# Kernel optimization log

Hardware: AMD Instinct MI355X
Metric: run time of the kernel (lower is better)

## Reference

```python
import jax, jax.numpy as jnp
import numpy as np

OUT_FEATURES = 4096
IN_FEATURES = 4096
GROUP_SIZE = 32
NUM_GROUPS = (OUT_FEATURES * IN_FEATURES) // GROUP_SIZE  # 524288, divisible by 8
PACKED_PER_GROUP = GROUP_SIZE * 3 // 8  # 12


def dequantize_3bit(x_packed, maxvals):
    # x_packed: [NUM_GROUPS * 12] int, values in [0,256) (uint8 bit patterns)
    # maxvals:  [NUM_GROUPS] float32 group scales
    G = NUM_GROUPS
    # view as [G, 4, 3]: 4 byte-triplets per group, each encoding 8 3-bit values
    p = x_packed.reshape(G, GROUP_SIZE // 8, 3)
    b0, b1, b2 = p[..., 0], p[..., 1], p[..., 2]
    v0 = b0 & 7
    v1 = (b0 >> 3) & 7
    v2 = ((b0 >> 6) & 3) | ((b1 & 1) << 2)
    v3 = (b1 >> 1) & 7
    v4 = (b1 >> 4) & 7
    v5 = ((b1 >> 7) & 1) | ((b2 & 3) << 1)
    v6 = (b2 >> 2) & 7
    v7 = (b2 >> 5) & 7
    q = jnp.stack([v0, v1, v2, v3, v4, v5, v6, v7], axis=-1)  # [G, 4, 8]
    q = q.reshape(G, GROUP_SIZE).astype(jnp.float32)
    x_norm = (q / 7.0 * 2.0 - 1.0) * maxvals[:, None]
    return x_norm.reshape(-1)  # [G * GROUP_SIZE]


def setup_inputs() -> dict:
    key = jax.random.key(0)
    k1, k2, k3, k4 = jax.random.split(key, 4)
    x = jax.random.normal(k1, (2, 2048, IN_FEATURES), dtype=jnp.float32)
    weight_q3 = jax.random.randint(k2, (NUM_GROUPS * PACKED_PER_GROUP,), 0, 256, dtype=jnp.int32)
    weight_norm = jax.random.uniform(k3, (NUM_GROUPS,), dtype=jnp.float32)
    bias = jax.random.normal(k4, (OUT_FEATURES,), dtype=jnp.float32)
    return {"x": x, "weight_q3": weight_q3, "weight_norm": weight_norm, "bias": bias}


def reference(x, weight_q3, weight_norm, bias):
    w_flat = dequantize_3bit(weight_q3, weight_norm)
    weight = w_flat[: OUT_FEATURES * IN_FEATURES].reshape(OUT_FEATURES, IN_FEATURES)
    # F.linear: y = x @ W.T + b
    return jnp.einsum("bsi,oi->bso", x, weight) + bias
```

## Files before the change

### kernel.cpp

```cpp
#include <hip/hip_runtime.h>

typedef unsigned short u16;
typedef unsigned int u32;

typedef __bf16 bf16x8 __attribute__((ext_vector_type(8)));
typedef float f32x4 __attribute__((ext_vector_type(4)));

#define OUT_F 4096
#define IN_F 4096
#define M_ROWS 4096
#define NUM_GROUPS ((OUT_F * IN_F) / 32)

#define TILE_E (256 * 64)


__device__ __forceinline__ u16 f2bf(float f) {
    union { float f; u32 u; } c; c.f = f;
    u32 u = c.u;
    u += 0x7fffu + ((u >> 16) & 1u);
    return (u16)(u >> 16);
}

__device__ __forceinline__ u32 pk2(float a, float b) {
    return (u32)f2bf(a) | ((u32)f2bf(b) << 16);
}

__device__ __forceinline__ void async_copy16(const u16* g, u16* l) {
    __builtin_amdgcn_global_load_lds(
        (const __attribute__((address_space(1))) u32*)g,
        (__attribute__((address_space(3))) u32*)l,
        16, 0, 0);
}

__device__ __forceinline__ u32 lds_addr(const u16* p) {
    return (u32)(uintptr_t)(const __attribute__((address_space(3))) u16*)p;
}

__global__ __launch_bounds__(256) void prep_kernel(
        const float* __restrict__ x, const int* __restrict__ q,
        const float* __restrict__ scales,
        u16* __restrict__ W, u16* __restrict__ Xb) {
    int bid = blockIdx.x;
    int tid = threadIdx.x;
    if (bid < 8192) {
        int t = bid * 256 + tid;
        int b0 = q[3 * t];
        int b1 = q[3 * t + 1];
        int b2 = q[3 * t + 2];
        float mv = scales[t >> 2];
        float s = mv * (2.0f / 7.0f);
        float o = -mv;

        int v0 = b0 & 7;
        int v1 = (b0 >> 3) & 7;
        int v2 = ((b0 >> 6) & 3) | ((b1 & 1) << 2);
        int v3 = (b1 >> 1) & 7;
        int v4 = (b1 >> 4) & 7;
        int v5 = ((b1 >> 7) & 1) | ((b2 & 3) << 1);
        int v6 = (b2 >> 2) & 7;
        int v7 = (b2 >> 5) & 7;
        uint4 w;
        w.x = pk2(fmaf((float)v0, s, o), fmaf((float)v1, s, o));
        w.y = pk2(fmaf((float)v2, s, o), fmaf((float)v3, s, o));
        w.z = pk2(fmaf((float)v4, s, o), fmaf((float)v5, s, o));
        w.w = pk2(fmaf((float)v6, s, o), fmaf((float)v7, s, o));
        ((uint4*)W)[t] = w;
    } else {
        int i = (bid - 8192) * 256 + tid;
        const float4* p = (const float4*)x + (size_t)i * 2;
        float4 u = p[0], v = p[1];
        uint4 w;
        w.x = pk2(u.x, u.y);
        w.y = pk2(u.z, u.w);
        w.z = pk2(v.x, v.y);
        w.w = pk2(v.z, v.w);
        ((uint4*)Xb)[i] = w;
    }
}

__global__ __launch_bounds__(512, 2) void gemm_bt_kernel(
        const u16* __restrict__ A, const u16* __restrict__ B,
        const float* __restrict__ bias, float* __restrict__ C) {
    __shared__ u16 sA[2 * TILE_E];
    __shared__ u16 sB[2 * TILE_E];

    const int tid = threadIdx.x;
    const int lane = tid & 63;
    const int w = tid >> 6;
    const int wr = w >> 2;
    const int wc = w & 3;
    const int ln = lane & 15;
    const int quad = lane >> 4;
    const int lnx = ln & 7;

    const int lin = blockIdx.x;
    const int wg = (lin & 7) * 32 + (lin >> 3);
    const int mb = (wg >> 4) * 256;
    const int nb = (wg & 15) * 256;

    int offg[2], offl[2];
#pragma unroll
    for (int p = 0; p < 2; ++p) {
        int s = p * 512 + tid;
        int rl = s >> 3, pc = s & 7;
        int lc = pc ^ (rl & 7);
        offg[p] = rl * IN_F + lc * 8;
        offl[p] = rl * 64 + pc * 8;
    }
    const u16* baseA = A + (size_t)mb * IN_F;
    const u16* baseB = B + (size_t)nb * IN_F;

    auto STAGE = [&](u16* lbase, const u16* gbase, int ko, int h) {
#pragma unroll
        for (int p = 0; p < 2; ++p)
            async_copy16(gbase + h * (128 * IN_F) + offg[p] + ko,
                         lbase + h * (128 * 64) + offl[p]);
    };

    const u32 sAb = lds_addr(sA);
    const u32 sBb = lds_addr(sB);
    const u32 aB0 = sAb + (u32)(wr * 8192 + ln * 128 + ((quad ^ lnx) * 16));
    const u32 aB1 = sAb + (u32)(wr * 8192 + ln * 128 + (((4 + quad) ^ lnx) * 16));
    const u32 bB0 = sBb + (u32)(wc * 4096 + ln * 128 + ((quad ^ lnx) * 16));
    const u32 bB1 = sBb + (u32)(wc * 4096 + ln * 128 + (((4 + quad) ^ lnx) * 16));

    float bj[2][2];
#pragma unroll
    for (int nh = 0; nh < 2; ++nh)
#pragma unroll
        for (int j = 0; j < 2; ++j)
            bj[nh][j] = bias[nb + nh * 128 + wc * 32 + j * 16 + ln];

    f32x4 acc[8][4];
#pragma unroll
    for (int i = 0; i < 8; ++i)
#pragma unroll
        for (int j = 0; j < 4; ++j) acc[i][j] = (f32x4)0.0f;

    bf16x8 av[4][2];
    bf16x8 bv0[2][2];
    bf16x8 bv1[2][2];

#define DSR(dst, base, IMM) \
    asm volatile("ds_read_b128 %0, %1 offset:" #IMM \
                 : "=v"(dst) : "v"(base))

#define WAITG(N) \
    asm volatile("s_waitcnt lgkmcnt(" #N ")"); \
    __builtin_amdgcn_sched_barrier(0);

#define MG(AI, ACR, J0, J1, BV) \
    acc[ACR][J0] = __builtin_amdgcn_mfma_f32_16x16x32_bf16( \
        av[AI][0], BV[0][0], acc[ACR][J0], 0, 0, 0); \
    acc[ACR][J0] = __builtin_amdgcn_mfma_f32_16x16x32_bf16( \
        av[AI][1], BV[0][1], acc[ACR][J0], 0, 0, 0); \
    acc[ACR][J1] = __builtin_amdgcn_mfma_f32_16x16x32_bf16( \
        av[AI][0], BV[1][0], acc[ACR][J1], 0, 0, 0); \
    acc[ACR][J1] = __builtin_amdgcn_mfma_f32_16x16x32_bf16( \
        av[AI][1], BV[1][1], acc[ACR][J1], 0, 0, 0);

    STAGE(sA, baseA, 0, 0);
    STAGE(sA, baseA, 0, 1);
    STAGE(sB, baseB, 0, 0);
    STAGE(sB, baseB, 0, 1);
    asm volatile("s_waitcnt vmcnt(0)");
    __builtin_amdgcn_s_barrier();

#pragma unroll 1
    for (int t = 0; t < 64; ++t) {
        const int cur = t & 1;
        const u32 curOff = (u32)cur << 15;
        const u32 aC0 = aB0 + curOff, aC1 = aB1 + curOff;
        const u32 bC0 = bB0 + curOff, bC1 = bB1 + curOff;
        u16* aNx = sA + (cur ^ 1) * TILE_E;
        u16* bNx = sB + (cur ^ 1) * TILE_E;
        const int ko1 = ((t + 1) & 63) << 6;

        DSR(bv0[0][0], bC0, 0);      DSR(bv0[0][1], bC1, 0);
        DSR(bv0[1][0], bC0, 2048);   DSR(bv0[1][1], bC1, 2048);
        DSR(av[0][0], aC0, 0);       DSR(av[0][1], aC1, 0);
        DSR(av[1][0], aC0, 2048);    DSR(av[1][1], aC1, 2048);
        DSR(av[2][0], aC0, 4096);    DSR(av[2][1], aC1, 4096);
        DSR(av[3][0], aC0, 6144);    DSR(av[3][1], aC1, 6144);
        DSR(bv1[0][0], bC0, 16384);  DSR(bv1[0][1], bC1, 16384);
        DSR(bv1[1][0], bC0, 18432);  DSR(bv1[1][1], bC1, 18432);

        STAGE(aNx, baseA, ko1, 0);
        STAGE(aNx, baseA, ko1, 1);
        STAGE(bNx, baseB, ko1, 0);
        STAGE(bNx, baseB, ko1, 1);
        __builtin_amdgcn_sched_barrier(0);

        __builtin_amdgcn_s_setprio(1);
        WAITG(10); MG(0, 0, 0, 1, bv0);
        WAITG(8);  MG(1, 1, 0, 1, bv0);
        WAITG(6);  MG(2, 2, 0, 1, bv0);
        WAITG(4);  MG(3, 3, 0, 1, bv0);
        WAITG(0);
        MG(0, 0, 2, 3, bv1);
        MG(1, 1, 2, 3, bv1);
        MG(2, 2, 2, 3, bv1);
        MG(3, 3, 2, 3, bv1);
        __builtin_amdgcn_sched_barrier(0);
        __builtin_amdgcn_s_setprio(0);

        DSR(av[0][0], aC0, 16384);   DSR(av[0][1], aC1, 16384);
        DSR(av[1][0], aC0, 18432);   DSR(av[1][1], aC1, 18432);
        DSR(av[2][0], aC0, 20480);   DSR(av[2][1], aC1, 20480);
        DSR(av[3][0], aC0, 22528);   DSR(av[3][1], aC1, 22528);

        __builtin_amdgcn_s_setprio(1);
        WAITG(6); MG(0, 4, 2, 3, bv1);
        WAITG(4); MG(1, 5, 2, 3, bv1);
        WAITG(2); MG(2, 6, 2, 3, bv1);
        WAITG(0); MG(3, 7, 2, 3, bv1);
        MG(0, 4, 0, 1, bv0);
        MG(1, 5, 0, 1, bv0);
        MG(2, 6, 0, 1, bv0);
        MG(3, 7, 0, 1, bv0);
        __builtin_amdgcn_sched_barrier(0);
        __builtin_amdgcn_s_setprio(0);

        asm volatile("s_waitcnt vmcnt(0)");
        __builtin_amdgcn_s_barrier();
    }

#undef DSR
#undef WAITG
#undef MG

    asm volatile("s_waitcnt vmcnt(0)");

#pragma unroll
    for (int ai = 0; ai < 8; ++ai) {
        const int mh = ai >> 2, i = ai & 3;
        const int mrow = mb + mh * 128 + wr * 64 + i * 16 + quad * 4;
#pragma unroll
        for (int j4 = 0; j4 < 4; ++j4) {
            const int nh = j4 >> 1, j = j4 & 1;
            const int col = nb + nh * 128 + wc * 32 + j * 16 + ln;
            float* cp = C + (size_t)mrow * OUT_F + col;
#pragma unroll
            for (int r = 0; r < 4; ++r)
                cp[(size_t)r * OUT_F] = acc[ai][j4][r] + bj[nh][j];
        }
    }
}

extern "C" void kernel_launch(void* const* d_in, const int* in_sizes, int n_in,
                              void* d_out, int out_size, void* d_ws, size_t ws_size,
                              hipStream_t stream) {
    const float* x = (const float*)d_in[0];
    const int* wq = (const int*)d_in[1];
    const float* wn = (const float*)d_in[2];
    const float* bias = (const float*)d_in[3];
    float* out = (float*)d_out;

    u16* Wb = (u16*)d_ws;
    u16* Xb = Wb + (size_t)OUT_F * IN_F;

    prep_kernel<<<16384, 256, 0, stream>>>(x, wq, wn, Wb, Xb);
    gemm_bt_kernel<<<dim3(256), 512, 0, stream>>>(Xb, Wb, bias, out);
}
```

Measured before the change: 141.3 us.

## Switch GEMM inner loop from 16x16x32 to 32x32x16 bf16 MFMA tiles

Replaces the 16x16x32 MFMA micro-tiles with 32x32x16 MFMA instructions. Each wave now owns a contiguous 128x64 output block as 4x2 accumulators of 16 floats. The LDS read addressing is rewritten to match the existing XOR swizzle, and K is processed in four 16-wide steps using two ping-pong register sets. The aim is fewer LDS reads per FLOP, since each 32x32 fragment gets more reuse, and fewer MFMA issues. The cost is a different store pattern in the epilogue and a risk of LDS bank conflicts or changed register pressure.

```diff
diff --git a/kernel.cpp b/kernel.cpp
--- a/kernel.cpp
+++ b/kernel.cpp
@@ -4,7 +4,7 @@
 typedef unsigned int u32;
 
 typedef __bf16 bf16x8 __attribute__((ext_vector_type(8)));
-typedef float f32x4 __attribute__((ext_vector_type(4)));
+typedef float f32x16 __attribute__((ext_vector_type(16)));
 
 #define OUT_F 4096
 #define IN_F 4096
@@ -89,9 +89,11 @@
     const int w = tid >> 6;
     const int wr = w >> 2;
     const int wc = w & 3;
-    const int ln = lane & 15;
-    const int quad = lane >> 4;
-    const int lnx = ln & 7;
+    const int l31 = lane & 31;
+    const int hi = lane >> 5;
+    const int l7 = lane & 7;
+    const int l72 = (l7 >> 1) & 3;
+    const int lb0 = l7 & 1;
 
     const int lin = blockIdx.x;
     const int wg = (lin & 7) * 32 + (lin >> 3);
@@ -119,27 +121,28 @@
 
     const u32 sAb = lds_addr(sA);
     const u32 sBb = lds_addr(sB);
-    const u32 aB0 = sAb + (u32)(wr * 8192 + ln * 128 + ((quad ^ lnx) * 16));
-    const u32 aB1 = sAb + (u32)(wr * 8192 + ln * 128 + (((4 + quad) ^ lnx) * 16));
-    const u32 bB0 = sBb + (u32)(wc * 4096 + ln * 128 + ((quad ^ lnx) * 16));
-    const u32 bB1 = sBb + (u32)(wc * 4096 + ln * 128 + (((4 + quad) ^ lnx) * 16));
-
-    float bj[2][2];
-#pragma unroll
-    for (int nh = 0; nh < 2; ++nh)
-#pragma unroll
-        for (int j = 0; j < 2; ++j)
-            bj[nh][j] = bias[nb + nh * 128 + wc * 32 + j * 16 + ln];
-
-    f32x4 acc[8][4];
-#pragma unroll
-    for (int i = 0; i < 8; ++i)
-#pragma unroll
-        for (int j = 0; j < 4; ++j) acc[i][j] = (f32x4)0.0f;
-
-    bf16x8 av[4][2];
-    bf16x8 bv0[2][2];
-    bf16x8 bv1[2][2];
+    const u32 aS = sAb + (u32)((wr * 128 + l31) * 128 + 16 * (hi ^ lb0));
+    const u32 bS = sBb + (u32)((wc * 64 + l31) * 128 + 16 * (hi ^ lb0));
+    u32 aK[4], bK[4];
+#pragma unroll
+    for (int ks = 0; ks < 4; ++ks) {
+        aK[ks] = aS + (u32)(32 * (ks ^ l72));
+        bK[ks] = bS + (u32)(32 * (ks ^ l72));
+    }
+
+    float bj[2];
+#pragma unroll
+    for (int cb = 0; cb < 2; ++cb)
+        bj[cb] = bias[nb + wc * 64 + cb * 32 + l31];
+
+    f32x16 acc[4][2];
+#pragma unroll
+    for (int rb = 0; rb < 4; ++rb)
+#pragma unroll
+        for (int cb = 0; cb < 2; ++cb) acc[rb][cb] = (f32x16)0.0f;
+
+    bf16x8 avE[4], bvE[2];
+    bf16x8 avO[4], bvO[2];
 
 #define DSR(dst, base, IMM) \
     asm volatile("ds_read_b128 %0, %1 offset:" #IMM \
@@ -149,15 +152,20 @@
     asm volatile("s_waitcnt lgkmcnt(" #N ")"); \
     __builtin_amdgcn_sched_barrier(0);
 
-#define MG(AI, ACR, J0, J1, BV) \
-    acc[ACR][J0] = __builtin_amdgcn_mfma_f32_16x16x32_bf16( \
-        av[AI][0], BV[0][0], acc[ACR][J0], 0, 0, 0); \
-    acc[ACR][J0] = __builtin_amdgcn_mfma_f32_16x16x32_bf16( \
-        av[AI][1], BV[0][1], acc[ACR][J0], 0, 0, 0); \
-    acc[ACR][J1] = __builtin_amdgcn_mfma_f32_16x16x32_bf16( \
-        av[AI][0], BV[1][0], acc[ACR][J1], 0, 0, 0); \
-    acc[ACR][J1] = __builtin_amdgcn_mfma_f32_16x16x32_bf16( \
-        av[AI][1], BV[1][1], acc[ACR][J1], 0, 0, 0);
+#define MFMA_K(AV, BV) \
+    acc[0][0] = __builtin_amdgcn_mfma_f32_32x32x16_bf16(AV[0], BV[0], acc[0][0], 0, 0, 0); \
+    acc[1][0] = __builtin_amdgcn_mfma_f32_32x32x16_bf16(AV[1], BV[0], acc[1][0], 0, 0, 0); \
+    acc[2][0] = __builtin_amdgcn_mfma_f32_32x32x16_bf16(AV[2], BV[0], acc[2][0], 0, 0, 0); \
+    acc[3][0] = __builtin_amdgcn_mfma_f32_32x32x16_bf16(AV[3], BV[0], acc[3][0], 0, 0, 0); \
+    acc[0][1] = __builtin_amdgcn_mfma_f32_32x32x16_bf16(AV[0], BV[1], acc[0][1], 0, 0, 0); \
+    acc[1][1] = __builtin_amdgcn_mfma_f32_32x32x16_bf16(AV[1], BV[1], acc[1][1], 0, 0, 0); \
+    acc[2][1] = __builtin_amdgcn_mfma_f32_32x32x16_bf16(AV[2], BV[1], acc[2][1], 0, 0, 0); \
+    acc[3][1] = __builtin_amdgcn_mfma_f32_32x32x16_bf16(AV[3], BV[1], acc[3][1], 0, 0, 0);
+
+#define READ_K(AV, BV, AT, BT) \
+    DSR(AV[0], AT, 0);  DSR(AV[1], AT, 4096); \
+    DSR(AV[2], AT, 8192); DSR(AV[3], AT, 12288); \
+    DSR(BV[0], BT, 0);  DSR(BV[1], BT, 4096);
 
     STAGE(sA, baseA, 0, 0);
     STAGE(sA, baseA, 0, 1);
@@ -170,20 +178,16 @@
     for (int t = 0; t < 64; ++t) {
         const int cur = t & 1;
         const u32 curOff = (u32)cur << 15;
-        const u32 aC0 = aB0 + curOff, aC1 = aB1 + curOff;
-        const u32 bC0 = bB0 + curOff, bC1 = bB1 + curOff;
+        const u32 aT0 = aK[0] + curOff, aT1 = aK[1] + curOff;
+        const u32 aT2 = aK[2] + curOff, aT3 = aK[3] + curOff;
+        const u32 bT0 = bK[0] + curOff, bT1 = bK[1] + curOff;
+        const u32 bT2 = bK[2] + curOff, bT3 = bK[3] + curOff;
         u16* aNx = sA + (cur ^ 1) * TILE_E;
         u16* bNx = sB + (cur ^ 1) * TILE_E;
         const int ko1 = ((t + 1) & 63) << 6;
 
-        DSR(bv0[0][0], bC0, 0);      DSR(bv0[0][1], bC1, 0);
-        DSR(bv0[1][0], bC0, 2048);   DSR(bv0[1][1], bC1, 2048);
-        DSR(av[0][0], aC0, 0);       DSR(av[0][1], aC1, 0);
-        DSR(av[1][0], aC0, 2048);    DSR(av[1][1], aC1, 2048);
-        DSR(av[2][0], aC0, 4096);    DSR(av[2][1], aC1, 4096);
-        DSR(av[3][0], aC0, 6144);    DSR(av[3][1], aC1, 6144);
-        DSR(bv1[0][0], bC0, 16384);  DSR(bv1[0][1], bC1, 16384);
-        DSR(bv1[1][0], bC0, 18432);  DSR(bv1[1][1], bC1, 18432);
+        READ_K(avE, bvE, aT0, bT0);
+        READ_K(avO, bvO, aT1, bT1);
 
         STAGE(aNx, baseA, ko1, 0);
         STAGE(aNx, baseA, ko1, 1);
@@ -192,32 +196,22 @@
         __builtin_amdgcn_sched_barrier(0);
 
         __builtin_amdgcn_s_setprio(1);
-        WAITG(10); MG(0, 0, 0, 1, bv0);
-        WAITG(8);  MG(1, 1, 0, 1, bv0);
-        WAITG(6);  MG(2, 2, 0, 1, bv0);
-        WAITG(4);  MG(3, 3, 0, 1, bv0);
-        WAITG(0);
-        MG(0, 0, 2, 3, bv1);
-        MG(1, 1, 2, 3, bv1);
-        MG(2, 2, 2, 3, bv1);
-        MG(3, 3, 2, 3, bv1);
+        WAITG(6); MFMA_K(avE, bvE);
         __builtin_amdgcn_sched_barrier(0);
         __builtin_amdgcn_s_setprio(0);
 
-        DSR(av[0][0], aC0, 16384);   DSR(av[0][1], aC1, 16384);
-        DSR(av[1][0], aC0, 18432);   DSR(av[1][1], aC1, 18432);
-        DSR(av[2][0], aC0, 20480);   DSR(av[2][1], aC1, 20480);
-        DSR(av[3][0], aC0, 22528);   DSR(av[3][1], aC1, 22528);
+        READ_K(avE, bvE, aT2, bT2);
 
         __builtin_amdgcn_s_setprio(1);
-        WAITG(6); MG(0, 4, 2, 3, bv1);
-        WAITG(4); MG(1, 5, 2, 3, bv1);
-        WAITG(2); MG(2, 6, 2, 3, bv1);
-        WAITG(0); MG(3, 7, 2, 3, bv1);
-        MG(0, 4, 0, 1, bv0);
-        MG(1, 5, 0, 1, bv0);
-        MG(2, 6, 0, 1, bv0);
-        MG(3, 7, 0, 1, bv0);
+        WAITG(6); MFMA_K(avO, bvO);
+        __builtin_amdgcn_sched_barrier(0);
+        __builtin_amdgcn_s_setprio(0);
+
+        READ_K(avO, bvO, aT3, bT3);
+
+        __builtin_amdgcn_s_setprio(1);
+        WAITG(6); MFMA_K(avE, bvE);
+        WAITG(0); MFMA_K(avO, bvO);
         __builtin_amdgcn_sched_barrier(0);
         __builtin_amdgcn_s_setprio(0);
 
@@ -227,22 +221,23 @@
 
 #undef DSR
 #undef WAITG
-#undef MG
+#undef MFMA_K
+#undef READ_K
 
     asm volatile("s_waitcnt vmcnt(0)");
 
 #pragma unroll
-    for (int ai = 0; ai < 8; ++ai) {
-        const int mh = ai >> 2, i = ai & 3;
-        const int mrow = mb + mh * 128 + wr * 64 + i * 16 + quad * 4;
-#pragma unroll
-        for (int j4 = 0; j4 < 4; ++j4) {
-            const int nh = j4 >> 1, j = j4 & 1;
-            const int col = nb + nh * 128 + wc * 32 + j * 16 + ln;
-            float* cp = C + (size_t)mrow * OUT_F + col;
-#pragma unroll
-            for (int r = 0; r < 4; ++r)
-                cp[(size_t)r * OUT_F] = acc[ai][j4][r] + bj[nh][j];
+    for (int rb = 0; rb < 4; ++rb) {
+        const int m0 = mb + wr * 128 + rb * 32 + 4 * hi;
+#pragma unroll
+        for (int cb = 0; cb < 2; ++cb) {
+            const int col = nb + wc * 64 + cb * 32 + l31;
+            const float bc = bj[cb];
+#pragma unroll
+            for (int r = 0; r < 16; ++r) {
+                const int row = m0 + (r & 3) + 8 * (r >> 2);
+                C[(size_t)row * OUT_F + col] = acc[rb][cb][r] + bc;
+            }
         }
     }
 }
```

Result: slower. 146.6 us (+3.7%).

## Software-pipeline LDS fragment reads across K-tiles with unrolled ping-pong buffers

Applied to the files above, without the earlier changes.

The GEMM main loop is unrolled by two with compile-time ping-pong LDS buffer addresses. The first B and A fragments of the next K-tile are loaded right after the barrier and overlap with the last MFMA group of the current tile. Separate register sets for the A halves and B fragments add VGPR pressure, which at launch bounds 512,2 risks spills. The extra barrier per iteration also adds synchronisation cost.

```diff
diff --git a/kernel.cpp b/kernel.cpp
--- a/kernel.cpp
+++ b/kernel.cpp
@@ -119,10 +119,15 @@
 
     const u32 sAb = lds_addr(sA);
     const u32 sBb = lds_addr(sB);
-    const u32 aB0 = sAb + (u32)(wr * 8192 + ln * 128 + ((quad ^ lnx) * 16));
-    const u32 aB1 = sAb + (u32)(wr * 8192 + ln * 128 + (((4 + quad) ^ lnx) * 16));
-    const u32 bB0 = sBb + (u32)(wc * 4096 + ln * 128 + ((quad ^ lnx) * 16));
-    const u32 bB1 = sBb + (u32)(wc * 4096 + ln * 128 + (((4 + quad) ^ lnx) * 16));
+    const u32 aX0 = sAb + (u32)(wr * 8192 + ln * 128 + ((quad ^ lnx) * 16));
+    const u32 aX1 = sAb + (u32)(wr * 8192 + ln * 128 + (((4 + quad) ^ lnx) * 16));
+    const u32 bX0 = sBb + (u32)(wc * 4096 + ln * 128 + ((quad ^ lnx) * 16));
+    const u32 bX1 = sBb + (u32)(wc * 4096 + ln * 128 + (((4 + quad) ^ lnx) * 16));
+    const u32 aY0 = aX0 + 32768, aY1 = aX1 + 32768;
+    const u32 bY0 = bX0 + 32768, bY1 = bX1 + 32768;
+
+    u16* const sA0 = sA;            u16* const sA1 = sA + TILE_E;
+    u16* const sB0 = sB;            u16* const sB1 = sB + TILE_E;
 
     float bj[2][2];
 #pragma unroll
@@ -137,9 +142,11 @@
 #pragma unroll
         for (int j = 0; j < 4; ++j) acc[i][j] = (f32x4)0.0f;
 
-    bf16x8 av[4][2];
-    bf16x8 bv0[2][2];
-    bf16x8 bv1[2][2];
+    bf16x8 a0v[4][2];
+    bf16x8 a1v[4][2];
+    bf16x8 b1v[2][2];
+    bf16x8 b0x[2][2];
+    bf16x8 b0y[2][2];
 
 #define DSR(dst, base, IMM) \
     asm volatile("ds_read_b128 %0, %1 offset:" #IMM \
@@ -149,87 +156,104 @@
     asm volatile("s_waitcnt lgkmcnt(" #N ")"); \
     __builtin_amdgcn_sched_barrier(0);
 
-#define MG(AI, ACR, J0, J1, BV) \
+#define MG(AV, AI, ACR, J0, J1, BV) \
     acc[ACR][J0] = __builtin_amdgcn_mfma_f32_16x16x32_bf16( \
-        av[AI][0], BV[0][0], acc[ACR][J0], 0, 0, 0); \
+        AV[AI][0], BV[0][0], acc[ACR][J0], 0, 0, 0); \
     acc[ACR][J0] = __builtin_amdgcn_mfma_f32_16x16x32_bf16( \
-        av[AI][1], BV[0][1], acc[ACR][J0], 0, 0, 0); \
+        AV[AI][1], BV[0][1], acc[ACR][J0], 0, 0, 0); \
     acc[ACR][J1] = __builtin_amdgcn_mfma_f32_16x16x32_bf16( \
-        av[AI][0], BV[1][0], acc[ACR][J1], 0, 0, 0); \
+        AV[AI][0], BV[1][0], acc[ACR][J1], 0, 0, 0); \
     acc[ACR][J1] = __builtin_amdgcn_mfma_f32_16x16x32_bf16( \
-        av[AI][1], BV[1][1], acc[ACR][J1], 0, 0, 0);
-
-    STAGE(sA, baseA, 0, 0);
-    STAGE(sA, baseA, 0, 1);
-    STAGE(sB, baseB, 0, 0);
-    STAGE(sB, baseB, 0, 1);
+        AV[AI][1], BV[1][1], acc[ACR][J1], 0, 0, 0);
+
+#define TILE_ITER(AB0, AB1, BB0, BB1, NA0, NA1, NB0, NB1, AWR, BWR, KO1, B0C, B0N) \
+    STAGE(AWR, baseA, KO1, 0); \
+    STAGE(AWR, baseA, KO1, 1); \
+    STAGE(BWR, baseB, KO1, 0); \
+    STAGE(BWR, baseB, KO1, 1); \
+    __builtin_amdgcn_sched_barrier(0); \
+     \
+    __builtin_amdgcn_s_setprio(1); \
+    WAITG(6); MG(a0v, 0, 0, 0, 1, B0C); \
+    WAITG(4); MG(a0v, 1, 1, 0, 1, B0C); \
+    WAITG(2); MG(a0v, 2, 2, 0, 1, B0C); \
+    WAITG(0); MG(a0v, 3, 3, 0, 1, B0C); \
+    __builtin_amdgcn_sched_barrier(0); \
+    __builtin_amdgcn_s_setprio(0); \
+     \
+    DSR(b1v[0][0], BB0, 16384);  DSR(b1v[0][1], BB1, 16384); \
+    DSR(b1v[1][0], BB0, 18432);  DSR(b1v[1][1], BB1, 18432); \
+    DSR(a1v[0][0], AB0, 16384);  DSR(a1v[0][1], AB1, 16384); \
+    DSR(a1v[1][0], AB0, 18432);  DSR(a1v[1][1], AB1, 18432); \
+    DSR(a1v[2][0], AB0, 20480);  DSR(a1v[2][1], AB1, 20480); \
+    DSR(a1v[3][0], AB0, 22528);  DSR(a1v[3][1], AB1, 22528); \
+    __builtin_amdgcn_sched_barrier(0); \
+     \
+    __builtin_amdgcn_s_setprio(1); \
+    WAITG(8); MG(a0v, 0, 0, 2, 3, b1v); \
+    MG(a0v, 1, 1, 2, 3, b1v); \
+    MG(a0v, 2, 2, 2, 3, b1v); \
+    MG(a0v, 3, 3, 2, 3, b1v); \
+    WAITG(6); MG(a1v, 0, 4, 2, 3, b1v); \
+    WAITG(4); MG(a1v, 1, 5, 2, 3, b1v); \
+    WAITG(2); MG(a1v, 2, 6, 2, 3, b1v); \
+    WAITG(0); MG(a1v, 3, 7, 2, 3, b1v); \
+    __builtin_amdgcn_sched_barrier(0); \
+    __builtin_amdgcn_s_setprio(0); \
+     \
+    asm volatile("s_waitcnt vmcnt(0)"); \
+    __builtin_amdgcn_s_barrier(); \
+     \
+    DSR(B0N[0][0], NB0, 0);     DSR(B0N[0][1], NB1, 0); \
+    DSR(B0N[1][0], NB0, 2048);  DSR(B0N[1][1], NB1, 2048); \
+    DSR(a0v[0][0], NA0, 0);     DSR(a0v[0][1], NA1, 0); \
+    DSR(a0v[1][0], NA0, 2048);  DSR(a0v[1][1], NA1, 2048); \
+    DSR(a0v[2][0], NA0, 4096);  DSR(a0v[2][1], NA1, 4096); \
+    DSR(a0v[3][0], NA0, 6144);  DSR(a0v[3][1], NA1, 6144); \
+    __builtin_amdgcn_sched_barrier(0); \
+     \
+    __builtin_amdgcn_s_setprio(1); \
+    MG(a1v, 0, 4, 0, 1, B0C); \
+    MG(a1v, 1, 5, 0, 1, B0C); \
+    MG(a1v, 2, 6, 0, 1, B0C); \
+    MG(a1v, 3, 7, 0, 1, B0C); \
+    __builtin_amdgcn_sched_barrier(0); \
+    __builtin_amdgcn_s_setprio(0); \
+     \
+    __builtin_amdgcn_s_barrier();
+
+    STAGE(sA0, baseA, 0, 0);
+    STAGE(sA0, baseA, 0, 1);
+    STAGE(sB0, baseB, 0, 0);
+    STAGE(sB0, baseB, 0, 1);
     asm volatile("s_waitcnt vmcnt(0)");
     __builtin_amdgcn_s_barrier();
+    DSR(b0x[0][0], bX0, 0);     DSR(b0x[0][1], bX1, 0);
+    DSR(b0x[1][0], bX0, 2048);  DSR(b0x[1][1], bX1, 2048);
+    DSR(a0v[0][0], aX0, 0);     DSR(a0v[0][1], aX1, 0);
+    DSR(a0v[1][0], aX0, 2048);  DSR(a0v[1][1], aX1, 2048);
+    DSR(a0v[2][0], aX0, 4096);  DSR(a0v[2][1], aX1, 4096);
+    DSR(a0v[3][0], aX0, 6144);  DSR(a0v[3][1], aX1, 6144);
+    __builtin_amdgcn_sched_barrier(0);
 
 #pragma unroll 1
-    for (int t = 0; t < 64; ++t) {
-        const int cur = t & 1;
-        const u32 curOff = (u32)cur << 15;
-        const u32 aC0 = aB0 + curOff, aC1 = aB1 + curOff;
-        const u32 bC0 = bB0 + curOff, bC1 = bB1 + curOff;
-        u16* aNx = sA + (cur ^ 1) * TILE_E;
-        u16* bNx = sB + (cur ^ 1) * TILE_E;
-        const int ko1 = ((t + 1) & 63) << 6;
-
-        DSR(bv0[0][0], bC0, 0);      DSR(bv0[0][1], bC1, 0);
-        DSR(bv0[1][0], bC0, 2048);   DSR(bv0[1][1], bC1, 2048);
-        DSR(av[0][0], aC0, 0);       DSR(av[0][1], aC1, 0);
-        DSR(av[1][0], aC0, 2048);    DSR(av[1][1], aC1, 2048);
-        DSR(av[2][0], aC0, 4096);    DSR(av[2][1], aC1, 4096);
-        DSR(av[3][0], aC0, 6144);    DSR(av[3][1], aC1, 6144);
-        DSR(bv1[0][0], bC0, 16384);  DSR(bv1[0][1], bC1, 16384);
-        DSR(bv1[1][0], bC0, 18432);  DSR(bv1[1][1], bC1, 18432);
-
-        STAGE(aNx, baseA, ko1, 0);
-        STAGE(aNx, baseA, ko1, 1);
-        STAGE(bNx, baseB, ko1, 0);
-        STAGE(bNx, baseB, ko1, 1);
-        __builtin_amdgcn_sched_barrier(0);
-
-        __builtin_amdgcn_s_setprio(1);
-        WAITG(10); MG(0, 0, 0, 1, bv0);
-        WAITG(8);  MG(1, 1, 0, 1, bv0);
-        WAITG(6);  MG(2, 2, 0, 1, bv0);
-        WAITG(4);  MG(3, 3, 0, 1, bv0);
-        WAITG(0);
-        MG(0, 0, 2, 3, bv1);
-        MG(1, 1, 2, 3, bv1);
-        MG(2, 2, 2, 3, bv1);
-        MG(3, 3, 2, 3, bv1);
-        __builtin_amdgcn_sched_barrier(0);
-        __builtin_amdgcn_s_setprio(0);
-
-        DSR(av[0][0], aC0, 16384);   DSR(av[0][1], aC1, 16384);
-        DSR(av[1][0], aC0, 18432);   DSR(av[1][1], aC1, 18432);
-        DSR(av[2][0], aC0, 20480);   DSR(av[2][1], aC1, 20480);
-        DSR(av[3][0], aC0, 22528);   DSR(av[3][1], aC1, 22528);
-
-        __builtin_amdgcn_s_setprio(1);
-        WAITG(6); MG(0, 4, 2, 3, bv1);
-        WAITG(4); MG(1, 5, 2, 3, bv1);
-        WAITG(2); MG(2, 6, 2, 3, bv1);
-        WAITG(0); MG(3, 7, 2, 3, bv1);
-        MG(0, 4, 0, 1, bv0);
-        MG(1, 5, 0, 1, bv0);
-        MG(2, 6, 0, 1, bv0);
-        MG(3, 7, 0, 1, bv0);
-        __builtin_amdgcn_sched_barrier(0);
-        __builtin_amdgcn_s_setprio(0);
-
-        asm volatile("s_waitcnt vmcnt(0)");
-        __builtin_amdgcn_s_barrier();
+    for (int tp = 0; tp < 32; ++tp) {
+        const int ko1e = ((2 * tp + 1) & 63) << 6;
+        const int ko1o = ((2 * tp + 2) & 63) << 6;
+        TILE_ITER(aX0, aX1, bX0, bX1, aY0, aY1, bY0, bY1,
+                  sA1, sB1, ko1e, b0x, b0y);
+        TILE_ITER(aY0, aY1, bY0, bY1, aX0, aX1, bX0, bX1,
+                  sA0, sB0, ko1o, b0y, b0x);
     }
 
 #undef DSR
 #undef WAITG
 #undef MG
-
+#undef TILE_ITER
+
+    asm volatile("s_waitcnt lgkmcnt(0)");
     asm volatile("s_waitcnt vmcnt(0)");
+    __builtin_amdgcn_sched_barrier(0);
 
 #pragma unroll
     for (int ai = 0; ai < 8; ++ai) {
```

Measured after the change: 143.0 us. No clear change (+1.2%).
